# Optimization experiments

Hardware: AMD Instinct MI355X
Metric: run time of the kernel (lower is better)

## Reference

```python
import jax, jax.numpy as jnp
import numpy as np

N_NODES = 50000
N_EDGES = 800000
IN_FEATS = 128
N_HIDDEN = 64
OUT_FEATS = 40
DIM = 8  # pseudo-coordinate dimension
K = 1    # n_kernels


def setup_inputs() -> dict:
    key = jax.random.key(0)
    ks = jax.random.split(key, 12)
    inp = {
        "features": jax.random.normal(ks[0], (N_NODES, IN_FEATS), dtype=jnp.float32),
        "edge_weight": jax.random.normal(ks[1], (N_EDGES, DIM), dtype=jnp.float32),
        "src": jax.random.randint(ks[2], (N_EDGES,), 0, N_NODES),
        "dst": jax.random.randint(ks[3], (N_EDGES,), 0, N_NODES),
        # layer 1 params (fc has no bias in DGL GMMConv; separate additive bias)
        "W1": jax.random.normal(ks[4], (IN_FEATS, K * N_HIDDEN), dtype=jnp.float32) * (1.0 / np.sqrt(IN_FEATS)),
        "b1": jnp.zeros((N_HIDDEN,), dtype=jnp.float32),
        "mu1": jax.random.normal(ks[5], (K, DIM), dtype=jnp.float32) * 0.1,
        "inv_sigma1": jnp.ones((K, DIM), dtype=jnp.float32),
        # layer 2 params
        "W2": jax.random.normal(ks[6], (N_HIDDEN, K * OUT_FEATS), dtype=jnp.float32) * (1.0 / np.sqrt(N_HIDDEN)),
        "b2": jnp.zeros((OUT_FEATS,), dtype=jnp.float32),
        "mu2": jax.random.normal(ks[7], (K, DIM), dtype=jnp.float32) * 0.1,
        "inv_sigma2": jnp.ones((K, DIM), dtype=jnp.float32),
    }
    return inp


def gmm_conv(x, pseudo, src, dst, W, b, mu, inv_sigma, out_feats):
    # x: [N, in], pseudo: [E, DIM], W: [in, K*out]
    h = (x @ W).reshape(-1, K, out_feats)                      # [N, K, out]
    # gaussian mixture weights per edge/kernel: [E, K]
    diff = pseudo[:, None, :] - mu[None, :, :]                 # [E, K, DIM]
    gw = jnp.exp(-0.5 * jnp.sum(diff * diff * (inv_sigma[None] ** 2), axis=-1))
    # gather src feats, weight, sum over kernels: [E, out]
    msg = jnp.einsum("ekf,ek->ef", h[src], gw)
    agg = jax.ops.segment_sum(msg, dst, num_segments=N_NODES)  # [N, out]
    return agg + b


def reference(features, edge_weight, src, dst, W1, b1, mu1, inv_sigma1, W2, b2, mu2, inv_sigma2):
    x = gmm_conv(features, edge_weight, src, dst, W1, b1, mu1, inv_sigma1, N_HIDDEN)
    x = gmm_conv(x, edge_weight, src, dst, W2, b2, mu2, inv_sigma2, OUT_FEATS)
    return jax.nn.log_softmax(x, axis=1)
```

## Files before the change

kernel.cpp:

```cpp
#include <hip/hip_runtime.h>
#include <hip/hip_fp16.h>
#include <math.h>

#define N_NODES 50000
#define N_EDGES 800000
#define IN_FEATS 128
#define N_HIDDEN 64
#define OUT_FEATS 40
#define DIM 8
#define GT_TILES ((N_NODES + 63) / 64)
#define HIST_NB ((N_EDGES / 4 + 255) / 256)
#define FILL_BLOCKS (N_EDGES / 256)
#define SCAN_NB ((N_NODES + 255) / 256)
#define CNT_STRIDE 4
#define WCOLS 48
#define W12_NB ((WCOLS * IN_FEATS) / 256)

typedef _Float16 half8 __attribute__((ext_vector_type(8)));
typedef float floatx4 __attribute__((ext_vector_type(4)));

__device__ __forceinline__ int wave_incl_scan(int x, int lane) {
#pragma unroll
    for (int off = 1; off < 64; off <<= 1) {
        int v = __shfl_up(x, off, 64);
        if (lane >= off) x += v;
    }
    return x;
}

__global__ __launch_bounds__(256) void w12_kernel(const float* __restrict__ W1,
                                                  const float* __restrict__ W2,
                                                  const float* __restrict__ b1,
                                                  __half* __restrict__ w12T,
                                                  float* __restrict__ cvec,
                                                  int* __restrict__ counts,
                                                  int* __restrict__ partials) {
    const int gtid = blockIdx.x * 256 + threadIdx.x;

    for (int i = gtid; i < (N_NODES * CNT_STRIDE) / 4; i += W12_NB * 256)
        ((int4*)counts)[i] = make_int4(0, 0, 0, 0);
    if (gtid < 256) partials[gtid] = 0;

    const int c = gtid >> 7;
    const int i = gtid & 127;
    float s = 0.f;
    if (c < OUT_FEATS) {
#pragma unroll 8
        for (int k = 0; k < N_HIDDEN; ++k)
            s += W1[i * N_HIDDEN + k] * W2[k * OUT_FEATS + c];
    }
    w12T[gtid] = __float2half(s);
    if (gtid < OUT_FEATS) {
        float t = 0.f;
        for (int k = 0; k < N_HIDDEN; ++k)
            t += b1[k] * W2[k * OUT_FEATS + gtid];
        cvec[gtid] = t;
    }
}

__global__ __launch_bounds__(256) void histgemm_kernel(
    const float* __restrict__ features, const __half* __restrict__ w12T,
    const int* __restrict__ dst,
    int* __restrict__ counts, unsigned short* __restrict__ rank,
    __half* __restrict__ y)
{
    const int tid = threadIdx.x;
    __shared__ __align__(16) __half WT[WCOLS][136];

    if (blockIdx.x < HIST_NB) {
        int i = blockIdx.x * 256 + tid;
        if (i * 4 >= N_EDGES) return;
        int4 d = ((const int4*)dst)[i];
        ushort4 r;
        r.x = (unsigned short)atomicAdd(&counts[d.x * CNT_STRIDE], 1);
        r.y = (unsigned short)atomicAdd(&counts[d.y * CNT_STRIDE], 1);
        r.z = (unsigned short)atomicAdd(&counts[d.z * CNT_STRIDE], 1);
        r.w = (unsigned short)atomicAdd(&counts[d.w * CNT_STRIDE], 1);
        ((ushort4*)rank)[i] = r;
        return;
    }

    int nodeBase = (blockIdx.x - HIST_NB) * 64;
    for (int rep = 0; rep < (WCOLS * IN_FEATS) / 256; ++rep) {
        int idx = tid + rep * 256;
        WT[idx >> 7][idx & 127] = w12T[idx];
    }
    __syncthreads();

    int lane = tid & 63, w = tid >> 6;
    int m = lane & 15, quad = lane >> 4;
    int row = nodeBase + w * 16 + m;
    int rowc = (row < N_NODES) ? row : (N_NODES - 1);
    const float* fr = features + (size_t)rowc * IN_FEATS;

    floatx4 acc0 = {0.f,0.f,0.f,0.f}, acc1 = acc0, acc2 = acc0;
#pragma unroll
    for (int kc = 0; kc < 4; ++kc) {
        float4 fa = *(const float4*)(fr + kc * 32 + quad * 8);
        float4 fb = *(const float4*)(fr + kc * 32 + quad * 8 + 4);
        union { half8 v; __half2 h2[4]; } A;
        A.h2[0] = __floats2half2_rn(fa.x, fa.y);
        A.h2[1] = __floats2half2_rn(fa.z, fa.w);
        A.h2[2] = __floats2half2_rn(fb.x, fb.y);
        A.h2[3] = __floats2half2_rn(fb.z, fb.w);
        half8 b0 = *(const half8*)&WT[ 0 + m][kc * 32 + quad * 8];
        half8 b1 = *(const half8*)&WT[16 + m][kc * 32 + quad * 8];
        half8 b2 = *(const half8*)&WT[32 + m][kc * 32 + quad * 8];
        acc0 = __builtin_amdgcn_mfma_f32_16x16x32_f16(A.v, b0, acc0, 0, 0, 0);
        acc1 = __builtin_amdgcn_mfma_f32_16x16x32_f16(A.v, b1, acc1, 0, 0, 0);
        acc2 = __builtin_amdgcn_mfma_f32_16x16x32_f16(A.v, b2, acc2, 0, 0, 0);
    }
    int nodeRow = nodeBase + w * 16 + quad * 4;
#pragma unroll
    for (int r = 0; r < 4; ++r) {
        int n = nodeRow + r;
        if (n < N_NODES) {
            size_t base = (size_t)n * OUT_FEATS;
            y[base + m]      = __float2half(acc0[r]);
            y[base + m + 16] = __float2half(acc1[r]);
            if (m < 8)
                y[base + m + 32] = __float2half(acc2[r]);
        }
    }
}

__global__ __launch_bounds__(256) void scan_kernel(const int* __restrict__ counts,
                                                   int* __restrict__ offsets,
                                                   int* __restrict__ partials) {
    const int tid = threadIdx.x, bid = blockIdx.x;
    const int i = bid * 256 + tid;
    const int lane = tid & 63, wid = tid >> 6;
    int x = (i < N_NODES) ? counts[i * CNT_STRIDE] : 0;
    int incl = wave_incl_scan(x, lane);
    __shared__ int wsum[4];
    __shared__ int sExc, sTot;
    if (lane == 63) wsum[wid] = incl;
    __syncthreads();
    int base = 0;
#pragma unroll
    for (int w = 0; w < 4; ++w)
        if (w < wid) base += wsum[w];
    int lexcl = base + incl - x;
    if (tid == 255) sTot = base + incl;
    __syncthreads();
    if (tid == 0) {
        int T = sTot;
        if (bid == 0) {
            __hip_atomic_store(&partials[0], (T << 2) | 2,
                               __ATOMIC_RELAXED, __HIP_MEMORY_SCOPE_AGENT);
            sExc = 0;
        } else {
            __hip_atomic_store(&partials[bid], (T << 2) | 1,
                               __ATOMIC_RELAXED, __HIP_MEMORY_SCOPE_AGENT);
            int sum = 0, pb = bid - 1;
            while (true) {
                int v = __hip_atomic_load(&partials[pb],
                                          __ATOMIC_RELAXED, __HIP_MEMORY_SCOPE_AGENT);
                if (v == 0) continue;
                sum += v >> 2;
                if ((v & 3) == 2) break;
                --pb;
            }
            __hip_atomic_store(&partials[bid], ((sum + T) << 2) | 2,
                               __ATOMIC_RELAXED, __HIP_MEMORY_SCOPE_AGENT);
            sExc = sum;
        }
    }
    __syncthreads();
    if (i < N_NODES) offsets[i] = sExc + lexcl;
    if (bid == SCAN_NB - 1 && tid == 0) offsets[N_NODES] = N_EDGES;
}

__global__ __launch_bounds__(256) void fill_kernel(
    const int* __restrict__ src, const int* __restrict__ dst,
    const float* __restrict__ ew,
    const float* __restrict__ mu1, const float* __restrict__ is1,
    const float* __restrict__ mu2, const float* __restrict__ is2,
    const int* __restrict__ offsets, const unsigned short* __restrict__ rank,
    int2* __restrict__ csr)
{
    int e = blockIdx.x * 256 + threadIdx.x;
    int sN = src[e];
    int dN = dst[e];
    unsigned short rk = rank[e];
    const float4* ew4 = (const float4*)(ew + (size_t)e * DIM);
    float4 wa = ew4[0], wb = ew4[1];
    float v[8] = {wa.x, wa.y, wa.z, wa.w, wb.x, wb.y, wb.z, wb.w};
    float s1 = 0.f, s2 = 0.f;
#pragma unroll
    for (int d = 0; d < DIM; ++d) {
        float d1 = v[d] - mu1[d]; float a1 = is1[d];
        float d2 = v[d] - mu2[d]; float a2 = is2[d];
        s1 += d1 * d1 * a1 * a1;
        s2 += d2 * d2 * a2 * a2;
    }
    __half2 g = __floats2half2_rn(expf(-0.5f * s1), expf(-0.5f * s2));
    int2 rec;
    rec.x = sN;
    rec.y = *reinterpret_cast<int*>(&g);
    int pos = offsets[dN] + rk;
    __builtin_nontemporal_store(*reinterpret_cast<long long*>(&rec),
                                reinterpret_cast<long long*>(&csr[pos]));
}

__global__ __launch_bounds__(256) void agg1_kernel(const __half* __restrict__ ysrc,
                                                   const int* __restrict__ offsets,
                                                   const int2* __restrict__ csr,
                                                   const float* __restrict__ cvec,
                                                   __half* __restrict__ h2) {
    const unsigned* h32 = (const unsigned*)ysrc;
    const int tid = threadIdx.x;
    const int w = tid >> 6, lane = tid & 63;
    const int hf = lane >> 5, p = lane & 31;
    const int n = blockIdx.x * 8 + w * 2 + hf;
    const int pc = (p < 20) ? p : 19;
    int beg = offsets[n], end = offsets[n + 1];

    float ax = 0.f, ay = 0.f;
    for (int j = beg; j < end; j += 8) {
        int j0 = j + 0, j1 = j + 1, j2 = j + 2, j3 = j + 3;
        int j4 = j + 4, j5 = j + 5, j6 = j + 6, j7 = j + 7;
        int e1 = end - 1;
        int2 r0 = csr[(j0 < end) ? j0 : e1];
        int2 r1 = csr[(j1 < end) ? j1 : e1];
        int2 r2 = csr[(j2 < end) ? j2 : e1];
        int2 r3 = csr[(j3 < end) ? j3 : e1];
        int2 r4 = csr[(j4 < end) ? j4 : e1];
        int2 r5 = csr[(j5 < end) ? j5 : e1];
        int2 r6 = csr[(j6 < end) ? j6 : e1];
        int2 r7 = csr[(j7 < end) ? j7 : e1];
        unsigned v0 = h32[(size_t)r0.x * 20 + pc];
        unsigned v1 = h32[(size_t)r1.x * 20 + pc];
        unsigned v2 = h32[(size_t)r2.x * 20 + pc];
        unsigned v3 = h32[(size_t)r3.x * 20 + pc];
        unsigned v4 = h32[(size_t)r4.x * 20 + pc];
        unsigned v5 = h32[(size_t)r5.x * 20 + pc];
        unsigned v6 = h32[(size_t)r6.x * 20 + pc];
        unsigned v7 = h32[(size_t)r7.x * 20 + pc];
        float g0 = (j0 < end) ? __low2float(*reinterpret_cast<__half2*>(&r0.y)) : 0.f;
        float g1 = (j1 < end) ? __low2float(*reinterpret_cast<__half2*>(&r1.y)) : 0.f;
        float g2 = (j2 < end) ? __low2float(*reinterpret_cast<__half2*>(&r2.y)) : 0.f;
        float g3 = (j3 < end) ? __low2float(*reinterpret_cast<__half2*>(&r3.y)) : 0.f;
        float g4 = (j4 < end) ? __low2float(*reinterpret_cast<__half2*>(&r4.y)) : 0.f;
        float g5 = (j5 < end) ? __low2float(*reinterpret_cast<__half2*>(&r5.y)) : 0.f;
        float g6 = (j6 < end) ? __low2float(*reinterpret_cast<__half2*>(&r6.y)) : 0.f;
        float g7 = (j7 < end) ? __low2float(*reinterpret_cast<__half2*>(&r7.y)) : 0.f;
        float2 f0 = __half22float2(*reinterpret_cast<__half2*>(&v0));
        float2 f1 = __half22float2(*reinterpret_cast<__half2*>(&v1));
        float2 f2 = __half22float2(*reinterpret_cast<__half2*>(&v2));
        float2 f3 = __half22float2(*reinterpret_cast<__half2*>(&v3));
        float2 f4 = __half22float2(*reinterpret_cast<__half2*>(&v4));
        float2 f5 = __half22float2(*reinterpret_cast<__half2*>(&v5));
        float2 f6 = __half22float2(*reinterpret_cast<__half2*>(&v6));
        float2 f7 = __half22float2(*reinterpret_cast<__half2*>(&v7));
        ax += f0.x * g0; ay += f0.y * g0;
        ax += f1.x * g1; ay += f1.y * g1;
        ax += f2.x * g2; ay += f2.y * g2;
        ax += f3.x * g3; ay += f3.y * g3;
        ax += f4.x * g4; ay += f4.y * g4;
        ax += f5.x * g5; ay += f5.y * g5;
        ax += f6.x * g6; ay += f6.y * g6;
        ax += f7.x * g7; ay += f7.y * g7;
    }
    if (p < 20) {
        __half2 hv = __floats2half2_rn(ax + cvec[2 * p], ay + cvec[2 * p + 1]);
        ((unsigned*)h2)[(size_t)n * 20 + p] = *reinterpret_cast<unsigned*>(&hv);
    }
}

__global__ __launch_bounds__(256) void agg2_kernel(const __half* __restrict__ h,
                                                   const int* __restrict__ offsets,
                                                   const int2* __restrict__ csr,
                                                   const float* __restrict__ b,
                                                   float* __restrict__ out) {
    const unsigned* h32 = (const unsigned*)h;
    const int tid = threadIdx.x;
    const int w = tid >> 6, lane = tid & 63;
    const int hf = lane >> 5, p = lane & 31;
    const int n = blockIdx.x * 8 + w * 2 + hf;
    const int pc = (p < 20) ? p : 19;
    int beg = offsets[n], end = offsets[n + 1];

    float ax = 0.f, ay = 0.f;
    for (int j = beg; j < end; j += 8) {
        int j0 = j + 0, j1 = j + 1, j2 = j + 2, j3 = j + 3;
        int j4 = j + 4, j5 = j + 5, j6 = j + 6, j7 = j + 7;
        int e1 = end - 1;
        int2 r0 = csr[(j0 < end) ? j0 : e1];
        int2 r1 = csr[(j1 < end) ? j1 : e1];
        int2 r2 = csr[(j2 < end) ? j2 : e1];
        int2 r3 = csr[(j3 < end) ? j3 : e1];
        int2 r4 = csr[(j4 < end) ? j4 : e1];
        int2 r5 = csr[(j5 < end) ? j5 : e1];
        int2 r6 = csr[(j6 < end) ? j6 : e1];
        int2 r7 = csr[(j7 < end) ? j7 : e1];
        unsigned v0 = h32[(size_t)r0.x * 20 + pc];
        unsigned v1 = h32[(size_t)r1.x * 20 + pc];
        unsigned v2 = h32[(size_t)r2.x * 20 + pc];
        unsigned v3 = h32[(size_t)r3.x * 20 + pc];
        unsigned v4 = h32[(size_t)r4.x * 20 + pc];
        unsigned v5 = h32[(size_t)r5.x * 20 + pc];
        unsigned v6 = h32[(size_t)r6.x * 20 + pc];
        unsigned v7 = h32[(size_t)r7.x * 20 + pc];
        float g0 = (j0 < end) ? __high2float(*reinterpret_cast<__half2*>(&r0.y)) : 0.f;
        float g1 = (j1 < end) ? __high2float(*reinterpret_cast<__half2*>(&r1.y)) : 0.f;
        float g2 = (j2 < end) ? __high2float(*reinterpret_cast<__half2*>(&r2.y)) : 0.f;
        float g3 = (j3 < end) ? __high2float(*reinterpret_cast<__half2*>(&r3.y)) : 0.f;
        float g4 = (j4 < end) ? __high2float(*reinterpret_cast<__half2*>(&r4.y)) : 0.f;
        float g5 = (j5 < end) ? __high2float(*reinterpret_cast<__half2*>(&r5.y)) : 0.f;
        float g6 = (j6 < end) ? __high2float(*reinterpret_cast<__half2*>(&r6.y)) : 0.f;
        float g7 = (j7 < end) ? __high2float(*reinterpret_cast<__half2*>(&r7.y)) : 0.f;
        float2 f0 = __half22float2(*reinterpret_cast<__half2*>(&v0));
        float2 f1 = __half22float2(*reinterpret_cast<__half2*>(&v1));
        float2 f2 = __half22float2(*reinterpret_cast<__half2*>(&v2));
        float2 f3 = __half22float2(*reinterpret_cast<__half2*>(&v3));
        float2 f4 = __half22float2(*reinterpret_cast<__half2*>(&v4));
        float2 f5 = __half22float2(*reinterpret_cast<__half2*>(&v5));
        float2 f6 = __half22float2(*reinterpret_cast<__half2*>(&v6));
        float2 f7 = __half22float2(*reinterpret_cast<__half2*>(&v7));
        ax += f0.x * g0; ay += f0.y * g0;
        ax += f1.x * g1; ay += f1.y * g1;
        ax += f2.x * g2; ay += f2.y * g2;
        ax += f3.x * g3; ay += f3.y * g3;
        ax += f4.x * g4; ay += f4.y * g4;
        ax += f5.x * g5; ay += f5.y * g5;
        ax += f6.x * g6; ay += f6.y * g6;
        ax += f7.x * g7; ay += f7.y * g7;
    }

    bool valid = (p < 20);
    float vx = valid ? ax + b[2 * p]     : -INFINITY;
    float vy = valid ? ay + b[2 * p + 1] : -INFINITY;
    float m = fmaxf(vx, vy);
#pragma unroll
    for (int off = 16; off; off >>= 1)
        m = fmaxf(m, __shfl_xor(m, off, 32));
    float ex = valid ? (expf(vx - m) + expf(vy - m)) : 0.f;
#pragma unroll
    for (int off = 16; off; off >>= 1)
        ex += __shfl_xor(ex, off, 32);
    float ls = logf(ex);
    if (valid) {
        float2 o = make_float2(vx - m - ls, vy - m - ls);
        *(float2*)&out[(size_t)n * OUT_FEATS + 2 * p] = o;
    }
}

extern "C" void kernel_launch(void* const* d_in, const int* in_sizes, int n_in,
                              void* d_out, int out_size, void* d_ws, size_t ws_size,
                              hipStream_t stream) {
    const float* features    = (const float*)d_in[0];
    const float* edge_weight = (const float*)d_in[1];
    const int*   src         = (const int*)d_in[2];
    const int*   dst         = (const int*)d_in[3];
    const float* W1          = (const float*)d_in[4];
    const float* b1          = (const float*)d_in[5];
    const float* mu1         = (const float*)d_in[6];
    const float* is1         = (const float*)d_in[7];
    const float* W2          = (const float*)d_in[8];
    const float* b2          = (const float*)d_in[9];
    const float* mu2         = (const float*)d_in[10];
    const float* is2         = (const float*)d_in[11];
    float* out = (float*)d_out;

    int2*           csr     = (int2*)d_ws;
    __half*         Y       = (__half*)(csr + N_EDGES);
    __half*         h2      = Y + (size_t)N_NODES * OUT_FEATS;
    int*            counts  = (int*)(h2 + (size_t)N_NODES * OUT_FEATS);
    unsigned short* rank    = (unsigned short*)(counts + N_NODES * CNT_STRIDE);
    int*            offsets = (int*)(rank + N_EDGES);
    int*            partials= offsets + N_NODES + 1;
    __half*         w12T    = (__half*)(partials + 256);
    float*          cvec    = (float*)(w12T + WCOLS * IN_FEATS);

    w12_kernel<<<W12_NB, 256, 0, stream>>>(W1, W2, b1, w12T, cvec, counts, partials);

    histgemm_kernel<<<HIST_NB + GT_TILES, 256, 0, stream>>>(
        features, w12T, dst, counts, rank, Y);

    scan_kernel<<<SCAN_NB, 256, 0, stream>>>(counts, offsets, partials);

    fill_kernel<<<FILL_BLOCKS, 256, 0, stream>>>(
        src, dst, edge_weight, mu1, is1, mu2, is2, offsets, rank, csr);

    agg1_kernel<<<N_NODES / 8, 256, 0, stream>>>(Y, offsets, csr, cvec, h2);

    agg2_kernel<<<N_NODES / 8, 256, 0, stream>>>(h2, offsets, csr, b2, out);
}
```

Baseline: 230.8 us.

## Move Gaussian weight computation into histogram/GEMM kernel and vectorize CSR fill

The per-edge Gaussian mixture weights are now computed in extra blocks of the fused histogram/GEMM launch and written to a temporary array. The fill kernel then only scatters records, with each thread handling four edges using vector loads. The aim is to overlap the edge-weight reads and exp math with the histogram atomics and GEMM work, and to make the post-scan fill phase cheaper. In exchange it adds a global round trip through the new weight array.

```diff
diff --git a/kernel.cpp b/kernel.cpp
--- a/kernel.cpp
+++ b/kernel.cpp
@@ -10,7 +10,8 @@
 #define DIM 8
 #define GT_TILES ((N_NODES + 63) / 64)
 #define HIST_NB ((N_EDGES / 4 + 255) / 256)
-#define FILL_BLOCKS (N_EDGES / 256)
+#define GAUSS_NB (N_EDGES / 256)
+#define FILLQ_NB ((N_EDGES / 4 + 255) / 256)
 #define SCAN_NB ((N_NODES + 255) / 256)
 #define CNT_STRIDE 4
 #define WCOLS 48
@@ -60,9 +61,11 @@
 
 __global__ __launch_bounds__(256) void histgemm_kernel(
     const float* __restrict__ features, const __half* __restrict__ w12T,
-    const int* __restrict__ dst,
+    const int* __restrict__ dst, const float* __restrict__ ew,
+    const float* __restrict__ mu1, const float* __restrict__ is1,
+    const float* __restrict__ mu2, const float* __restrict__ is2,
     int* __restrict__ counts, unsigned short* __restrict__ rank,
-    __half* __restrict__ y)
+    int* __restrict__ garr, __half* __restrict__ y)
 {
     const int tid = threadIdx.x;
     __shared__ __align__(16) __half WT[WCOLS][136];
@@ -80,7 +83,25 @@
         return;
     }
 
-    int nodeBase = (blockIdx.x - HIST_NB) * 64;
+    if (blockIdx.x < HIST_NB + GAUSS_NB) {
+        int e = (blockIdx.x - HIST_NB) * 256 + tid;
+        const float4* ew4 = (const float4*)(ew + (size_t)e * DIM);
+        float4 wa = ew4[0], wb = ew4[1];
+        float v[8] = {wa.x, wa.y, wa.z, wa.w, wb.x, wb.y, wb.z, wb.w};
+        float s1 = 0.f, s2 = 0.f;
+#pragma unroll
+        for (int d = 0; d < DIM; ++d) {
+            float d1 = v[d] - mu1[d]; float a1 = is1[d];
+            float d2 = v[d] - mu2[d]; float a2 = is2[d];
+            s1 += d1 * d1 * a1 * a1;
+            s2 += d2 * d2 * a2 * a2;
+        }
+        __half2 g = __floats2half2_rn(expf(-0.5f * s1), expf(-0.5f * s2));
+        garr[e] = *reinterpret_cast<int*>(&g);
+        return;
+    }
+
+    int nodeBase = (blockIdx.x - HIST_NB - GAUSS_NB) * 64;
     for (int rep = 0; rep < (WCOLS * IN_FEATS) / 256; ++rep) {
         int idx = tid + rep * 256;
         WT[idx >> 7][idx & 127] = w12T[idx];
@@ -173,34 +194,31 @@
 
 __global__ __launch_bounds__(256) void fill_kernel(
     const int* __restrict__ src, const int* __restrict__ dst,
-    const float* __restrict__ ew,
-    const float* __restrict__ mu1, const float* __restrict__ is1,
-    const float* __restrict__ mu2, const float* __restrict__ is2,
     const int* __restrict__ offsets, const unsigned short* __restrict__ rank,
-    int2* __restrict__ csr)
+    const int* __restrict__ garr, int2* __restrict__ csr)
 {
-    int e = blockIdx.x * 256 + threadIdx.x;
-    int sN = src[e];
-    int dN = dst[e];
-    unsigned short rk = rank[e];
-    const float4* ew4 = (const float4*)(ew + (size_t)e * DIM);
-    float4 wa = ew4[0], wb = ew4[1];
-    float v[8] = {wa.x, wa.y, wa.z, wa.w, wb.x, wb.y, wb.z, wb.w};
-    float s1 = 0.f, s2 = 0.f;
-#pragma unroll
-    for (int d = 0; d < DIM; ++d) {
-        float d1 = v[d] - mu1[d]; float a1 = is1[d];
-        float d2 = v[d] - mu2[d]; float a2 = is2[d];
-        s1 += d1 * d1 * a1 * a1;
-        s2 += d2 * d2 * a2 * a2;
-    }
-    __half2 g = __floats2half2_rn(expf(-0.5f * s1), expf(-0.5f * s2));
-    int2 rec;
-    rec.x = sN;
-    rec.y = *reinterpret_cast<int*>(&g);
-    int pos = offsets[dN] + rk;
-    __builtin_nontemporal_store(*reinterpret_cast<long long*>(&rec),
-                                reinterpret_cast<long long*>(&csr[pos]));
+    int q = blockIdx.x * 256 + threadIdx.x;
+    if (q * 4 >= N_EDGES) return;
+    int4    s4 = ((const int4*)src)[q];
+    int4    d4 = ((const int4*)dst)[q];
+    ushort4 r4 = ((const ushort4*)rank)[q];
+    int4    g4 = ((const int4*)garr)[q];
+    int p0 = offsets[d4.x] + r4.x;
+    int p1 = offsets[d4.y] + r4.y;
+    int p2 = offsets[d4.z] + r4.z;
+    int p3 = offsets[d4.w] + r4.w;
+    int2 rec0 = make_int2(s4.x, g4.x);
+    int2 rec1 = make_int2(s4.y, g4.y);
+    int2 rec2 = make_int2(s4.z, g4.z);
+    int2 rec3 = make_int2(s4.w, g4.w);
+    __builtin_nontemporal_store(*reinterpret_cast<long long*>(&rec0),
+                                reinterpret_cast<long long*>(&csr[p0]));
+    __builtin_nontemporal_store(*reinterpret_cast<long long*>(&rec1),
+                                reinterpret_cast<long long*>(&csr[p1]));
+    __builtin_nontemporal_store(*reinterpret_cast<long long*>(&rec2),
+                                reinterpret_cast<long long*>(&csr[p2]));
+    __builtin_nontemporal_store(*reinterpret_cast<long long*>(&rec3),
+                                reinterpret_cast<long long*>(&csr[p3]));
 }
 
 __global__ __launch_bounds__(256) void agg1_kernel(const __half* __restrict__ ysrc,
@@ -372,16 +390,17 @@
     int*            partials= offsets + N_NODES + 1;
     __half*         w12T    = (__half*)(partials + 256);
     float*          cvec    = (float*)(w12T + WCOLS * IN_FEATS);
+    int*            garr    = (int*)(cvec + 64);
 
     w12_kernel<<<W12_NB, 256, 0, stream>>>(W1, W2, b1, w12T, cvec, counts, partials);
 
-    histgemm_kernel<<<HIST_NB + GT_TILES, 256, 0, stream>>>(
-        features, w12T, dst, counts, rank, Y);
+    histgemm_kernel<<<HIST_NB + GAUSS_NB + GT_TILES, 256, 0, stream>>>(
+        features, w12T, dst, edge_weight, mu1, is1, mu2, is2,
+        counts, rank, garr, Y);
 
     scan_kernel<<<SCAN_NB, 256, 0, stream>>>(counts, offsets, partials);
 
-    fill_kernel<<<FILL_BLOCKS, 256, 0, stream>>>(
-        src, dst, edge_weight, mu1, is1, mu2, is2, offsets, rank, csr);
+    fill_kernel<<<FILLQ_NB, 256, 0, stream>>>(src, dst, offsets, rank, garr, csr);
 
     agg1_kernel<<<N_NODES / 8, 256, 0, stream>>>(Y, offsets, csr, cvec, h2);
 
```

Result: slower. 239.6 us (+3.8%).
